# Kernel tuning notes

Hardware: AMD Instinct MI355X
Metric: run time of the kernel (lower is better)

Reference implementation:

```python
import jax, jax.numpy as jnp
import numpy as np

D_MODEL = 2048
N_HEADS = 16
N_KV_HEADS = 4
HEAD_DIM = 128
ROPE_THETA = 10000.0


def _rope_cos_sin(T, hd, theta):
    # [T, hd//2]
    inv_freq = 1.0 / (theta ** (jnp.arange(0, hd, 2, dtype=jnp.float32) / hd))
    ang = jnp.arange(T, dtype=jnp.float32)[:, None] * inv_freq[None, :]
    return jnp.cos(ang), jnp.sin(ang)


def _apply_rope(x, cos, sin):
    # x: [B, H, T, hd]; rotate-half (Llama-style) RoPE
    hd = x.shape[-1]
    x1, x2 = x[..., : hd // 2], x[..., hd // 2 :]
    c = cos[None, None, :, :]
    s = sin[None, None, :, :]
    return jnp.concatenate([x1 * c - x2 * s, x2 * c + x1 * s], axis=-1)


def setup_inputs() -> dict:
    key = jax.random.key(0)
    ks = jax.random.split(key, 5)
    B, T = 2, 2048
    x = jax.random.normal(ks[0], (B, T, D_MODEL), dtype=jnp.float32)
    sq = 1.0 / np.sqrt(D_MODEL)
    Wq = jax.random.normal(ks[1], (D_MODEL, N_HEADS * HEAD_DIM), dtype=jnp.float32) * sq
    Wk = jax.random.normal(ks[2], (D_MODEL, N_KV_HEADS * HEAD_DIM), dtype=jnp.float32) * sq
    Wv = jax.random.normal(ks[3], (D_MODEL, N_KV_HEADS * HEAD_DIM), dtype=jnp.float32) * sq
    Wo = jax.random.normal(ks[4], (N_HEADS * HEAD_DIM, D_MODEL), dtype=jnp.float32) * sq
    return {"x": x, "Wq": Wq, "Wk": Wk, "Wv": Wv, "Wo": Wo}


def reference(x, Wq, Wk, Wv, Wo):
    B, T, _ = x.shape
    H, KV, hd = N_HEADS, N_KV_HEADS, HEAD_DIM
    n_rep = H // KV

    q = (x @ Wq).reshape(B, T, H, hd).transpose(0, 2, 1, 3)    # [B,H,T,hd]
    k = (x @ Wk).reshape(B, T, KV, hd).transpose(0, 2, 1, 3)   # [B,KV,T,hd]
    v = (x @ Wv).reshape(B, T, KV, hd).transpose(0, 2, 1, 3)

    cos, sin = _rope_cos_sin(T, hd, ROPE_THETA)
    q = _apply_rope(q, cos, sin)
    k = _apply_rope(k, cos, sin)

    # repeat KV heads for GQA: [B,KV,T,hd] -> [B,H,T,hd]
    k = jnp.repeat(k, n_rep, axis=1)
    v = jnp.repeat(v, n_rep, axis=1)

    scale = 1.0 / jnp.sqrt(jnp.float32(hd))
    scores = jnp.einsum("bhqd,bhkd->bhqk", q, k) * scale       # [B,H,T,T]
    causal = jnp.tril(jnp.ones((T, T), dtype=bool))
    scores = jnp.where(causal[None, None, :, :], scores, -jnp.inf)
    attn = jax.nn.softmax(scores, axis=-1)
    out = jnp.einsum("bhqk,bhkd->bhqd", attn, v)               # [B,H,T,hd]
    out = out.transpose(0, 2, 1, 3).reshape(B, T, H * hd)
    return out @ Wo
```

## Files before the change

kernel.cpp:

```cpp
#include <hip/hip_runtime.h>
#include <stdint.h>

#define T_SEQ 2048
#define DM    2048
#define NH    16
#define NKV   4
#define HD    128
#define MROWS 4096
#define NQKV  3072

typedef unsigned short u16;
typedef __bf16 bf16x8 __attribute__((ext_vector_type(8)));
typedef float  f32x4  __attribute__((ext_vector_type(4)));

__device__ __forceinline__ u16 f2b(float f) {
  union { float f; unsigned u; } v; v.f = f;
  return (u16)((v.u + 0x7fffu + ((v.u >> 16) & 1u)) >> 16);
}
__device__ __forceinline__ float b2f(u16 u) {
  union { unsigned u; float f; } v; v.u = ((unsigned)u) << 16;
  return v.f;
}
__device__ __forceinline__ void gl_lds16(const u16* g, u16* l) {
  __builtin_amdgcn_global_load_lds(
      (__attribute__((address_space(1))) void*)g,
      (__attribute__((address_space(3))) void*)l, 16, 0, 0);
}
__device__ __forceinline__ void storev(float* p, float v) { *p = v; }
__device__ __forceinline__ void storev(u16* p, float v)   { *p = f2b(v); }

__global__ __launch_bounds__(256) void k_cvt_x(const float* __restrict__ x,
                                               u16* __restrict__ o, int n) {
  int i = (blockIdx.x * 256 + threadIdx.x) * 4;
  if (i >= n) return;
  float4 v = *(const float4*)(x + i);
  ushort4 r;
  r.x = f2b(v.x); r.y = f2b(v.y); r.z = f2b(v.z); r.w = f2b(v.w);
  *(ushort4*)(o + i) = r;
}

__global__ __launch_bounds__(256) void k_tw4(const float* __restrict__ Wq,
                                             const float* __restrict__ Wk,
                                             const float* __restrict__ Wv,
                                             const float* __restrict__ Wo,
                                             u16* __restrict__ WT,
                                             u16* __restrict__ Wot) {
  __shared__ float tl[32][33];
  int z = blockIdx.z;
  const float* in; u16* out; int Nd, xt;
  if (z < 64)      { in = Wq; out = WT;               Nd = 2048; xt = z; }
  else if (z < 80) { in = Wk; out = WT + 2048 * 2048; Nd = 512;  xt = z - 64; }
  else if (z < 96) { in = Wv; out = WT + 2560 * 2048; Nd = 512;  xt = z - 80; }
  else             { in = Wo; out = Wot;              Nd = 2048; xt = z - 96; }
  int n0 = xt * 32, k0 = blockIdx.y * 32;
  int tx = threadIdx.x, ty = threadIdx.y;
#pragma unroll
  for (int i = 0; i < 32; i += 8)
    tl[ty + i][tx] = in[(long)(k0 + ty + i) * Nd + n0 + tx];
  __syncthreads();
#pragma unroll
  for (int i = 0; i < 32; i += 8)
    out[(long)(n0 + ty + i) * 2048 + k0 + tx] = f2b(tl[tx][ty + i]);
}

template <typename OutT>
__global__ __launch_bounds__(256) void k_gemm(const u16* __restrict__ A,
                                              const u16* __restrict__ Bt,
                                              OutT* __restrict__ C,
                                              int M, int N, int K) {
  __shared__ __align__(16) u16 As[128 * 32];
  __shared__ __align__(16) u16 Bs[128 * 32];
  const int tid = threadIdx.x;
  const int wv = tid >> 6, lane = tid & 63;
  const int quad = lane >> 4, ln = lane & 15;
  const int wm = wv & 1, wn = wv >> 1;
  const int rchnk = quad ^ ((ln >> 1) & 3);
  const long m0 = (long)blockIdx.x * 128;
  const long n0 = (long)blockIdx.y * 128;
  f32x4 acc[4][4] = {};
  for (int k0 = 0; k0 < K; k0 += 32) {
#pragma unroll
    for (int r = 0; r < 2; ++r) {
      int c = r * 256 + tid;
      int gc = (c & 3) ^ ((c >> 3) & 3);
      gl_lds16(A  + (m0 + (c >> 2)) * K + k0 + gc * 8, &As[(r * 256 + wv * 64) * 8]);
      gl_lds16(Bt + (n0 + (c >> 2)) * K + k0 + gc * 8, &Bs[(r * 256 + wv * 64) * 8]);
    }
    __syncthreads();
    bf16x8 af[4], bg[4];
#pragma unroll
    for (int i = 0; i < 4; ++i)
      af[i] = *(const bf16x8*)&As[(wm * 64 + i * 16 + ln) * 32 + rchnk * 8];
#pragma unroll
    for (int j = 0; j < 4; ++j)
      bg[j] = *(const bf16x8*)&Bs[(wn * 64 + j * 16 + ln) * 32 + rchnk * 8];
#pragma unroll
    for (int i = 0; i < 4; ++i)
#pragma unroll
      for (int j = 0; j < 4; ++j)
        acc[i][j] = __builtin_amdgcn_mfma_f32_16x16x32_bf16(af[i], bg[j], acc[i][j], 0, 0, 0);
    __syncthreads();
  }
#pragma unroll
  for (int i = 0; i < 4; ++i) {
    long row = m0 + wm * 64 + i * 16 + quad * 4;
#pragma unroll
    for (int j = 0; j < 4; ++j) {
      long col = n0 + wn * 64 + j * 16 + ln;
#pragma unroll
      for (int r = 0; r < 4; ++r)
        storev(&C[(row + r) * N + col], acc[i][j][r]);
    }
  }
}

__global__ __launch_bounds__(256) void k_rope2(const u16* __restrict__ C,
                                               u16* __restrict__ Qo,
                                               u16* __restrict__ Ko) {
  int idx = blockIdx.x * 256 + threadIdx.x;
  int d = idx & 63;
  int t = (idx >> 6) & (T_SEQ - 1);
  int g = idx >> 17;
  int b = (g >= 20) ? 1 : 0;
  int hh = g - b * 20;
  int isQ = hh < 16;
  int head = isQ ? hh : (hh - 16);
  int coloff = isQ ? 0 : 2048;
  float qscale = isQ ? 0.12751745f : 1.0f;
  u16* o = isQ ? Qo : Ko;
  int nh = isQ ? NH : NKV;
  long inb = (long)(b * T_SEQ + t) * NQKV + coloff + head * HD + d;
  float q1 = b2f(C[inb]);
  float q2 = b2f(C[inb + 64]);
  float inv = __expf(-0.14391156f * (float)d);
  float sn, cs;
  __sincosf((float)t * inv, &sn, &cs);
  long ob = (((long)b * nh + head) * T_SEQ + t) * HD + d;
  o[ob]      = f2b((q1 * cs - q2 * sn) * qscale);
  o[ob + 64] = f2b((q2 * cs + q1 * sn) * qscale);
}

__global__ __launch_bounds__(256) void k_vt(const u16* __restrict__ C,
                                            u16* __restrict__ Vt) {
  __shared__ u16 tl[32][33];
  int bkv = blockIdx.z;
  int t0 = blockIdx.x * 32, d0 = blockIdx.y * 32;
  int tx = threadIdx.x, ty = threadIdx.y;
  int b = bkv >> 2, kv = bkv & 3;
#pragma unroll
  for (int i = 0; i < 32; i += 8)
    tl[ty + i][tx] = C[(long)(b * T_SEQ + t0 + ty + i) * NQKV + 2560 + kv * HD + d0 + tx];
  __syncthreads();
#pragma unroll
  for (int i = 0; i < 32; i += 8)
    Vt[((long)bkv * HD + d0 + ty + i) * T_SEQ + t0 + tx] = tl[tx][ty + i];
}

template <bool DIAG>
__device__ __forceinline__ void p_emit(f32x4 (&S)[4], u16* __restrict__ Pb,
                                       int quad, int ln, int mrow) {
#pragma unroll
  for (int nt = 0; nt < 4; ++nt)
#pragma unroll
    for (int r = 0; r < 4; ++r) {
      float v = S[nt][r];
      if (DIAG) v = (nt * 16 + ln <= mrow + r) ? v : -1e30f;
      float pv = exp2f(v - 8.0f);
      int row = quad * 4 + r;
      int chnk = (nt * 2 + (ln >> 3)) ^ (row & 7);
      *(__bf16*)&Pb[row * 64 + chnk * 8 + (ln & 7)] = (__bf16)pv;
    }
}

__global__ __launch_bounds__(256, 2) void k_attn(const u16* __restrict__ Q,
                                                 const u16* __restrict__ Kg,
                                                 const u16* __restrict__ Vt,
                                                 u16* __restrict__ Og) {
  __shared__ __align__(16) u16 Ks[64 * 128];
  __shared__ __align__(16) u16 Vs[128 * 64];
  __shared__ __align__(16) u16 Ps[4][2][16 * 64];
  const int tid = threadIdx.x;
  const int wv = tid >> 6, lane = tid & 63;
  const int quad = lane >> 4, ln = lane & 15;
  const int bh = blockIdx.y;
  const int b = bh >> 4, h = bh & 15;
  const int kvh = h >> 2;
  const int p = blockIdx.x;
  const int thi = 31 - p, tlo = p;
  const int qhi = thi * 64 + wv * 16;
  const int qlo = tlo * 64 + wv * 16;

  bf16x8 qfh[4], qfl[4];
  {
    const u16* qp = Q + ((long)bh * T_SEQ + qhi + ln) * HD + quad * 8;
#pragma unroll
    for (int s = 0; s < 4; ++s) qfh[s] = *(const bf16x8*)(qp + s * 32);
    qp = Q + ((long)bh * T_SEQ + qlo + ln) * HD + quad * 8;
#pragma unroll
    for (int s = 0; s < 4; ++s) qfl[s] = *(const bf16x8*)(qp + s * 32);
  }
  bf16x8 onesb;
#pragma unroll
  for (int i = 0; i < 8; ++i) onesb[i] = (__bf16)1.0f;

  f32x4 lh = {0.f, 0.f, 0.f, 0.f}, ll = {0.f, 0.f, 0.f, 0.f};
  f32x4 oh[8] = {}, ol[8] = {};

  const u16* Kb = Kg + (long)(b * NKV + kvh) * T_SEQ * HD;
  const u16* Vb = Vt + (long)(b * NKV + kvh) * HD * T_SEQ;

  for (int kt = 0; kt <= thi; ++kt) {
    const int k0 = kt * 64;
#pragma unroll
    for (int r = 0; r < 4; ++r) {
      int s = r * 256 + tid;
      gl_lds16(Kb + (long)(k0 + (s >> 4)) * HD + (((s & 15) ^ ((s >> 4) & 15)) << 3),
               &Ks[(r * 256 + wv * 64) * 8]);
      gl_lds16(Vb + (long)(s >> 3) * T_SEQ + k0 + (((s & 7) ^ ((s >> 3) & 7)) << 3),
               &Vs[(r * 256 + wv * 64) * 8]);
    }
    __syncthreads();
    const bool lo_act = (kt <= tlo);
    f32x4 Sh[4], Sl[4];
#pragma unroll
    for (int nt = 0; nt < 4; ++nt) {
      bf16x8 kb[4];
      const u16* kp = &Ks[(nt * 16 + ln) * 128];
#pragma unroll
      for (int ss = 0; ss < 4; ++ss)
        kb[ss] = *(const bf16x8*)(kp + (((quad + 4 * ss) ^ ln) << 3));
      f32x4 s = {0.f, 0.f, 0.f, 0.f};
#pragma unroll
      for (int ss = 0; ss < 4; ++ss)
        s = __builtin_amdgcn_mfma_f32_16x16x32_bf16(qfh[ss], kb[ss], s, 0, 0, 0);
      Sh[nt] = s;
      if (lo_act) {
        f32x4 t = {0.f, 0.f, 0.f, 0.f};
#pragma unroll
        for (int ss = 0; ss < 4; ++ss)
          t = __builtin_amdgcn_mfma_f32_16x16x32_bf16(qfl[ss], kb[ss], t, 0, 0, 0);
        Sl[nt] = t;
      }
    }
    if (kt == thi) p_emit<true>(Sh, &Ps[wv][0][0], quad, ln, wv * 16 + quad * 4);
    else           p_emit<false>(Sh, &Ps[wv][0][0], quad, ln, 0);
    if (lo_act) {
      if (kt == tlo) p_emit<true>(Sl, &Ps[wv][1][0], quad, ln, wv * 16 + quad * 4);
      else           p_emit<false>(Sl, &Ps[wv][1][0], quad, ln, 0);
    }
    asm volatile("s_waitcnt lgkmcnt(0)" ::: "memory");
    bf16x8 pfh[2], pfl[2];
#pragma unroll
    for (int ss = 0; ss < 2; ++ss)
      pfh[ss] = *(const bf16x8*)&Ps[wv][0][ln * 64 + (((ss * 4 + quad) ^ (ln & 7)) << 3)];
    if (lo_act) {
#pragma unroll
      for (int ss = 0; ss < 2; ++ss)
        pfl[ss] = *(const bf16x8*)&Ps[wv][1][ln * 64 + (((ss * 4 + quad) ^ (ln & 7)) << 3)];
    }
    lh = __builtin_amdgcn_mfma_f32_16x16x32_bf16(pfh[0], onesb, lh, 0, 0, 0);
    lh = __builtin_amdgcn_mfma_f32_16x16x32_bf16(pfh[1], onesb, lh, 0, 0, 0);
    if (lo_act) {
      ll = __builtin_amdgcn_mfma_f32_16x16x32_bf16(pfl[0], onesb, ll, 0, 0, 0);
      ll = __builtin_amdgcn_mfma_f32_16x16x32_bf16(pfl[1], onesb, ll, 0, 0, 0);
    }
#pragma unroll
    for (int dt = 0; dt < 8; ++dt) {
      bf16x8 vb[2];
      const u16* vp = &Vs[(dt * 16 + ln) * 64];
#pragma unroll
      for (int ss = 0; ss < 2; ++ss)
        vb[ss] = *(const bf16x8*)(vp + (((quad + 4 * ss) ^ (ln & 7)) << 3));
#pragma unroll
      for (int ss = 0; ss < 2; ++ss)
        oh[dt] = __builtin_amdgcn_mfma_f32_16x16x32_bf16(pfh[ss], vb[ss], oh[dt], 0, 0, 0);
      if (lo_act) {
#pragma unroll
        for (int ss = 0; ss < 2; ++ss)
          ol[dt] = __builtin_amdgcn_mfma_f32_16x16x32_bf16(pfl[ss], vb[ss], ol[dt], 0, 0, 0);
      }
    }
    __syncthreads();
  }
  float rh[4], rl[4];
#pragma unroll
  for (int r = 0; r < 4; ++r) { rh[r] = 1.f / lh[r]; rl[r] = 1.f / ll[r]; }
#pragma unroll
  for (int dt = 0; dt < 8; ++dt)
#pragma unroll
    for (int r = 0; r < 4; ++r) {
      long rowh = (long)b * T_SEQ + qhi + quad * 4 + r;
      long rowl = (long)b * T_SEQ + qlo + quad * 4 + r;
      Og[rowh * (NH * HD) + h * HD + dt * 16 + ln] = f2b(oh[dt][r] * rh[r]);
      Og[rowl * (NH * HD) + h * HD + dt * 16 + ln] = f2b(ol[dt][r] * rl[r]);
    }
}

extern "C" void kernel_launch(void* const* d_in, const int* in_sizes, int n_in,
                              void* d_out, int out_size, void* d_ws, size_t ws_size,
                              hipStream_t stream) {
  const float* x  = (const float*)d_in[0];
  const float* Wq = (const float*)d_in[1];
  const float* Wk = (const float*)d_in[2];
  const float* Wv = (const float*)d_in[3];
  const float* Wo = (const float*)d_in[4];
  float* out = (float*)d_out;
  char* ws = (char*)d_ws;
  u16* WT  = (u16*)(ws + 0);
  u16* Wot = (u16*)(ws + 12582912);
  u16* Cq  = (u16*)(ws + 20971520);
  u16* Xb  = (u16*)(ws + 46137344);
  u16* Kb  = (u16*)(ws + 62914560);
  u16* Vtb = (u16*)(ws + 67108864);
  u16* Qb = Xb;
  u16* attn = Cq;

  k_cvt_x<<<8192, 256, 0, stream>>>(x, Xb, MROWS * DM);
  k_tw4<<<dim3(1, 64, 160), dim3(32, 8), 0, stream>>>(Wq, Wk, Wv, Wo, WT, Wot);

  k_gemm<u16><<<dim3(32, 24), 256, 0, stream>>>(Xb, WT, Cq, MROWS, NQKV, DM);

  k_rope2<<<20480, 256, 0, stream>>>(Cq, Qb, Kb);
  k_vt<<<dim3(64, 4, 8), dim3(32, 8), 0, stream>>>(Cq, Vtb);

  k_attn<<<dim3(16, 32), 256, 0, stream>>>(Qb, Kb, Vtb, attn);

  k_gemm<float><<<dim3(32, 16), 256, 0, stream>>>(attn, Wot, out, MROWS, DM, 2048);
}
```

Before: 314.3 us.

## Fuse RoPE into QKV GEMM epilogue, merge prep kernels, double-buffer attention KV

Merges the x conversion and weight transposes into one launch. Moves RoPE and the Q/K head-layout scatter into the QKV GEMM epilogue, with a column remap so each wave holds both rotate-half partners, and has V written head-major so a wider vectorized transpose can follow. In attention, K/V tiles are double-buffered so the next tile's global-to-LDS load overlaps compute, and MFMA sections get raised wave priority. This removes a launch and a full round-trip of the QKV intermediate, in exchange for more LDS per block and scattered epilogue stores.

```diff
diff --git a/kernel.cpp b/kernel.cpp
--- a/kernel.cpp
+++ b/kernel.cpp
@@ -29,31 +29,35 @@
 __device__ __forceinline__ void storev(float* p, float v) { *p = v; }
 __device__ __forceinline__ void storev(u16* p, float v)   { *p = f2b(v); }
 
-__global__ __launch_bounds__(256) void k_cvt_x(const float* __restrict__ x,
-                                               u16* __restrict__ o, int n) {
-  int i = (blockIdx.x * 256 + threadIdx.x) * 4;
-  if (i >= n) return;
-  float4 v = *(const float4*)(x + i);
-  ushort4 r;
-  r.x = f2b(v.x); r.y = f2b(v.y); r.z = f2b(v.z); r.w = f2b(v.w);
-  *(ushort4*)(o + i) = r;
-}
-
-__global__ __launch_bounds__(256) void k_tw4(const float* __restrict__ Wq,
+__global__ __launch_bounds__(256) void k_pre(const float* __restrict__ x,
+                                             const float* __restrict__ Wq,
                                              const float* __restrict__ Wk,
                                              const float* __restrict__ Wv,
                                              const float* __restrict__ Wo,
+                                             u16* __restrict__ Xb,
                                              u16* __restrict__ WT,
                                              u16* __restrict__ Wot) {
+  int bid = blockIdx.x;
+  int tid = threadIdx.x;
+  if (bid < 8192) {
+    int i = (bid * 256 + tid) * 4;
+    float4 v = *(const float4*)(x + i);
+    ushort4 r;
+    r.x = f2b(v.x); r.y = f2b(v.y); r.z = f2b(v.z); r.w = f2b(v.w);
+    *(ushort4*)(Xb + i) = r;
+    return;
+  }
   __shared__ float tl[32][33];
-  int z = blockIdx.z;
+  int zz = bid - 8192;
+  int z = zz >> 6;
+  int ky = zz & 63;
   const float* in; u16* out; int Nd, xt;
   if (z < 64)      { in = Wq; out = WT;               Nd = 2048; xt = z; }
   else if (z < 80) { in = Wk; out = WT + 2048 * 2048; Nd = 512;  xt = z - 64; }
   else if (z < 96) { in = Wv; out = WT + 2560 * 2048; Nd = 512;  xt = z - 80; }
   else             { in = Wo; out = Wot;              Nd = 2048; xt = z - 96; }
-  int n0 = xt * 32, k0 = blockIdx.y * 32;
-  int tx = threadIdx.x, ty = threadIdx.y;
+  int n0 = xt * 32, k0 = ky * 32;
+  int tx = tid & 31, ty = tid >> 5;
 #pragma unroll
   for (int i = 0; i < 32; i += 8)
     tl[ty + i][tx] = in[(long)(k0 + ty + i) * Nd + n0 + tx];
@@ -63,10 +67,13 @@
     out[(long)(n0 + ty + i) * 2048 + k0 + tx] = f2b(tl[tx][ty + i]);
 }
 
-template <typename OutT>
+template <int MODE, typename OutT>
 __global__ __launch_bounds__(256) void k_gemm(const u16* __restrict__ A,
                                               const u16* __restrict__ Bt,
                                               OutT* __restrict__ C,
+                                              u16* __restrict__ Qn,
+                                              u16* __restrict__ Kb,
+                                              u16* __restrict__ Vc,
                                               int M, int N, int K) {
   __shared__ __align__(16) u16 As[128 * 32];
   __shared__ __align__(16) u16 Bs[128 * 32];
@@ -93,7 +100,7 @@
       af[i] = *(const bf16x8*)&As[(wm * 64 + i * 16 + ln) * 32 + rchnk * 8];
 #pragma unroll
     for (int j = 0; j < 4; ++j)
-      bg[j] = *(const bf16x8*)&Bs[(wn * 64 + j * 16 + ln) * 32 + rchnk * 8];
+      bg[j] = *(const bf16x8*)&Bs[(wn * 32 + (j >> 1) * 64 + (j & 1) * 16 + ln) * 32 + rchnk * 8];
 #pragma unroll
     for (int i = 0; i < 4; ++i)
 #pragma unroll
@@ -101,59 +108,94 @@
         acc[i][j] = __builtin_amdgcn_mfma_f32_16x16x32_bf16(af[i], bg[j], acc[i][j], 0, 0, 0);
     __syncthreads();
   }
-#pragma unroll
-  for (int i = 0; i < 4; ++i) {
-    long row = m0 + wm * 64 + i * 16 + quad * 4;
-#pragma unroll
-    for (int j = 0; j < 4; ++j) {
-      long col = n0 + wn * 64 + j * 16 + ln;
-#pragma unroll
-      for (int r = 0; r < 4; ++r)
-        storev(&C[(row + r) * N + col], acc[i][j][r]);
-    }
-  }
-}
-
-__global__ __launch_bounds__(256) void k_rope2(const u16* __restrict__ C,
-                                               u16* __restrict__ Qo,
-                                               u16* __restrict__ Ko) {
-  int idx = blockIdx.x * 256 + threadIdx.x;
-  int d = idx & 63;
-  int t = (idx >> 6) & (T_SEQ - 1);
-  int g = idx >> 17;
-  int b = (g >= 20) ? 1 : 0;
-  int hh = g - b * 20;
-  int isQ = hh < 16;
-  int head = isQ ? hh : (hh - 16);
-  int coloff = isQ ? 0 : 2048;
-  float qscale = isQ ? 0.12751745f : 1.0f;
-  u16* o = isQ ? Qo : Ko;
-  int nh = isQ ? NH : NKV;
-  long inb = (long)(b * T_SEQ + t) * NQKV + coloff + head * HD + d;
-  float q1 = b2f(C[inb]);
-  float q2 = b2f(C[inb + 64]);
-  float inv = __expf(-0.14391156f * (float)d);
-  float sn, cs;
-  __sincosf((float)t * inv, &sn, &cs);
-  long ob = (((long)b * nh + head) * T_SEQ + t) * HD + d;
-  o[ob]      = f2b((q1 * cs - q2 * sn) * qscale);
-  o[ob + 64] = f2b((q2 * cs + q1 * sn) * qscale);
-}
-
-__global__ __launch_bounds__(256) void k_vt(const u16* __restrict__ C,
+  if constexpr (MODE == 0) {
+#pragma unroll
+    for (int i = 0; i < 4; ++i) {
+      long row = m0 + wm * 64 + i * 16 + quad * 4;
+#pragma unroll
+      for (int j = 0; j < 4; ++j) {
+        long col = n0 + wn * 32 + (j >> 1) * 64 + (j & 1) * 16 + ln;
+#pragma unroll
+        for (int r = 0; r < 4; ++r)
+          storev(&C[(row + r) * N + col], acc[i][j][r]);
+      }
+    }
+  } else {
+    const int nt = blockIdx.y;
+    if (nt < 20) {
+      const int isQ = nt < 16;
+      const int head = isQ ? nt : nt - 16;
+      u16* o = isQ ? Qn : Kb;
+      const int nh = isQ ? NH : NKV;
+      const float qs = isQ ? 0.12751745f : 1.0f;
+      const int d0 = wn * 32 + ln;
+      const float inv0 = __expf(-0.14391156f * (float)d0);
+      const float inv1 = __expf(-0.14391156f * (float)(d0 + 16));
+#pragma unroll
+      for (int i = 0; i < 4; ++i) {
+#pragma unroll
+        for (int r = 0; r < 4; ++r) {
+          long row = m0 + wm * 64 + i * 16 + quad * 4 + r;
+          int b = (int)(row >> 11), t = (int)(row & (T_SEQ - 1));
+          long ob = ((long)(b * nh + head) * T_SEQ + t) * HD;
+#pragma unroll
+          for (int j = 0; j < 2; ++j) {
+            int d = d0 + j * 16;
+            float q1 = acc[i][j][r], q2 = acc[i][j + 2][r];
+            float sn, cs;
+            __sincosf((float)t * (j ? inv1 : inv0), &sn, &cs);
+            o[ob + d]      = f2b((q1 * cs - q2 * sn) * qs);
+            o[ob + d + 64] = f2b((q2 * cs + q1 * sn) * qs);
+          }
+        }
+      }
+    } else {
+      const int kv = nt - 20;
+#pragma unroll
+      for (int i = 0; i < 4; ++i) {
+#pragma unroll
+        for (int r = 0; r < 4; ++r) {
+          long row = m0 + wm * 64 + i * 16 + quad * 4 + r;
+          int b = (int)(row >> 11), t = (int)(row & (T_SEQ - 1));
+          long ob = ((long)(b * NKV + kv) * T_SEQ + t) * HD;
+#pragma unroll
+          for (int j = 0; j < 4; ++j) {
+            int d = wn * 32 + (j >> 1) * 64 + (j & 1) * 16 + ln;
+            Vc[ob + d] = f2b(acc[i][j][r]);
+          }
+        }
+      }
+    }
+  }
+}
+
+__global__ __launch_bounds__(256) void k_vt(const u16* __restrict__ Vc,
                                             u16* __restrict__ Vt) {
-  __shared__ u16 tl[32][33];
+  __shared__ u16 tl[64][68];
   int bkv = blockIdx.z;
-  int t0 = blockIdx.x * 32, d0 = blockIdx.y * 32;
-  int tx = threadIdx.x, ty = threadIdx.y;
-  int b = bkv >> 2, kv = bkv & 3;
-#pragma unroll
-  for (int i = 0; i < 32; i += 8)
-    tl[ty + i][tx] = C[(long)(b * T_SEQ + t0 + ty + i) * NQKV + 2560 + kv * HD + d0 + tx];
+  int t0 = blockIdx.x * 64, d0 = blockIdx.y * 64;
+  int tx = threadIdx.x & 15, ty = threadIdx.x >> 4;
+  const u16* src = Vc + ((long)bkv * T_SEQ + t0) * HD + d0;
+#pragma unroll
+  for (int ii = 0; ii < 4; ++ii) {
+    ushort4 v = *(const ushort4*)&src[(ty + 16 * ii) * HD + tx * 4];
+    tl[ty + 16 * ii][tx * 4 + 0] = v.x;
+    tl[ty + 16 * ii][tx * 4 + 1] = v.y;
+    tl[ty + 16 * ii][tx * 4 + 2] = v.z;
+    tl[ty + 16 * ii][tx * 4 + 3] = v.w;
+  }
   __syncthreads();
-#pragma unroll
-  for (int i = 0; i < 32; i += 8)
-    Vt[((long)bkv * HD + d0 + ty + i) * T_SEQ + t0 + tx] = tl[tx][ty + i];
+  u16* dst = Vt + ((long)bkv * HD + d0) * T_SEQ + t0;
+#pragma unroll
+  for (int ii = 0; ii < 4; ++ii) {
+    int dr = ty + 16 * ii;
+    ushort4 o;
+    o.x = tl[tx * 4 + 0][dr];
+    o.y = tl[tx * 4 + 1][dr];
+    o.z = tl[tx * 4 + 2][dr];
+    o.w = tl[tx * 4 + 3][dr];
+    *(ushort4*)&dst[(long)dr * T_SEQ + tx * 4] = o;
+  }
 }
 
 template <bool DIAG>
@@ -176,8 +218,8 @@
                                                  const u16* __restrict__ Kg,
                                                  const u16* __restrict__ Vt,
                                                  u16* __restrict__ Og) {
-  __shared__ __align__(16) u16 Ks[64 * 128];
-  __shared__ __align__(16) u16 Vs[128 * 64];
+  __shared__ __align__(16) u16 Ks[2][64 * 128];
+  __shared__ __align__(16) u16 Vs[2][128 * 64];
   __shared__ __align__(16) u16 Ps[4][2][16 * 64];
   const int tid = threadIdx.x;
   const int wv = tid >> 6, lane = tid & 63;
@@ -209,23 +251,34 @@
   const u16* Kb = Kg + (long)(b * NKV + kvh) * T_SEQ * HD;
   const u16* Vb = Vt + (long)(b * NKV + kvh) * HD * T_SEQ;
 
-  for (int kt = 0; kt <= thi; ++kt) {
+  auto stageKV = [&](int kt, int idx) {
     const int k0 = kt * 64;
 #pragma unroll
     for (int r = 0; r < 4; ++r) {
       int s = r * 256 + tid;
       gl_lds16(Kb + (long)(k0 + (s >> 4)) * HD + (((s & 15) ^ ((s >> 4) & 15)) << 3),
-               &Ks[(r * 256 + wv * 64) * 8]);
+               &Ks[idx][(r * 256 + wv * 64) * 8]);
       gl_lds16(Vb + (long)(s >> 3) * T_SEQ + k0 + (((s & 7) ^ ((s >> 3) & 7)) << 3),
-               &Vs[(r * 256 + wv * 64) * 8]);
-    }
-    __syncthreads();
+               &Vs[idx][(r * 256 + wv * 64) * 8]);
+    }
+  };
+
+  stageKV(0, 0);
+  asm volatile("s_waitcnt vmcnt(0)" ::: "memory");
+  __builtin_amdgcn_s_barrier();
+
+  for (int kt = 0; kt <= thi; ++kt) {
+    const int cur = kt & 1;
+    if (kt < thi) stageKV(kt + 1, cur ^ 1);
+    const u16* Ksc = Ks[cur];
+    const u16* Vsc = Vs[cur];
     const bool lo_act = (kt <= tlo);
     f32x4 Sh[4], Sl[4];
+    __builtin_amdgcn_s_setprio(1);
 #pragma unroll
     for (int nt = 0; nt < 4; ++nt) {
       bf16x8 kb[4];
-      const u16* kp = &Ks[(nt * 16 + ln) * 128];
+      const u16* kp = &Ksc[(nt * 16 + ln) * 128];
 #pragma unroll
       for (int ss = 0; ss < 4; ++ss)
         kb[ss] = *(const bf16x8*)(kp + (((quad + 4 * ss) ^ ln) << 3));
@@ -242,6 +295,7 @@
         Sl[nt] = t;
       }
     }
+    __builtin_amdgcn_s_setprio(0);
     if (kt == thi) p_emit<true>(Sh, &Ps[wv][0][0], quad, ln, wv * 16 + quad * 4);
     else           p_emit<false>(Sh, &Ps[wv][0][0], quad, ln, 0);
     if (lo_act) {
@@ -258,6 +312,7 @@
       for (int ss = 0; ss < 2; ++ss)
         pfl[ss] = *(const bf16x8*)&Ps[wv][1][ln * 64 + (((ss * 4 + quad) ^ (ln & 7)) << 3)];
     }
+    __builtin_amdgcn_s_setprio(1);
     lh = __builtin_amdgcn_mfma_f32_16x16x32_bf16(pfh[0], onesb, lh, 0, 0, 0);
     lh = __builtin_amdgcn_mfma_f32_16x16x32_bf16(pfh[1], onesb, lh, 0, 0, 0);
     if (lo_act) {
@@ -267,7 +322,7 @@
 #pragma unroll
     for (int dt = 0; dt < 8; ++dt) {
       bf16x8 vb[2];
-      const u16* vp = &Vs[(dt * 16 + ln) * 64];
+      const u16* vp = &Vsc[(dt * 16 + ln) * 64];
 #pragma unroll
       for (int ss = 0; ss < 2; ++ss)
         vb[ss] = *(const bf16x8*)(vp + (((quad + 4 * ss) ^ (ln & 7)) << 3));
@@ -280,7 +335,9 @@
           ol[dt] = __builtin_amdgcn_mfma_f32_16x16x32_bf16(pfl[ss], vb[ss], ol[dt], 0, 0, 0);
       }
     }
-    __syncthreads();
+    __builtin_amdgcn_s_setprio(0);
+    asm volatile("s_waitcnt vmcnt(0)" ::: "memory");
+    __builtin_amdgcn_s_barrier();
   }
   float rh[4], rl[4];
 #pragma unroll
@@ -308,22 +365,22 @@
   char* ws = (char*)d_ws;
   u16* WT  = (u16*)(ws + 0);
   u16* Wot = (u16*)(ws + 12582912);
-  u16* Cq  = (u16*)(ws + 20971520);
+  u16* Vc  = (u16*)(ws + 20971520);
+  u16* Qn  = (u16*)(ws + 25165824);
   u16* Xb  = (u16*)(ws + 46137344);
   u16* Kb  = (u16*)(ws + 62914560);
   u16* Vtb = (u16*)(ws + 67108864);
-  u16* Qb = Xb;
-  u16* attn = Cq;
-
-  k_cvt_x<<<8192, 256, 0, stream>>>(x, Xb, MROWS * DM);
-  k_tw4<<<dim3(1, 64, 160), dim3(32, 8), 0, stream>>>(Wq, Wk, Wv, Wo, WT, Wot);
-
-  k_gemm<u16><<<dim3(32, 24), 256, 0, stream>>>(Xb, WT, Cq, MROWS, NQKV, DM);
-
-  k_rope2<<<20480, 256, 0, stream>>>(Cq, Qb, Kb);
-  k_vt<<<dim3(64, 4, 8), dim3(32, 8), 0, stream>>>(Cq, Vtb);
-
-  k_attn<<<dim3(16, 32), 256, 0, stream>>>(Qb, Kb, Vtb, attn);
-
-  k_gemm<float><<<dim3(32, 16), 256, 0, stream>>>(attn, Wot, out, MROWS, DM, 2048);
-}
+  u16* attn = Xb;
+
+  k_pre<<<18432, 256, 0, stream>>>(x, Wq, Wk, Wv, Wo, Xb, WT, Wot);
+
+  k_gemm<1, u16><<<dim3(32, 24), 256, 0, stream>>>(
+      Xb, WT, (u16*)nullptr, Qn, Kb, Vc, MROWS, NQKV, DM);
+
+  k_vt<<<dim3(32, 2, 8), 256, 0, stream>>>(Vc, Vtb);
+
+  k_attn<<<dim3(16, 32), 256, 0, stream>>>(Qn, Kb, Vtb, attn);
+
+  k_gemm<0, float><<<dim3(32, 16), 256, 0, stream>>>(
+      attn, Wot, out, nullptr, nullptr, nullptr, MROWS, DM, 2048);
+}
```

After: 306.4 us. -2.5%, faster.
